# Kernel tuning notes

Hardware: AMD Instinct MI355X
Metric: run time of the kernel (lower is better)

## Reference

```python
import jax, jax.numpy as jnp
import numpy as np

W_PRIOR_STD = 1.0          # w_prior_stddev
OBS_STD = 1.0              # observational_noise_stddev
EPS = 1e-7                 # keras backend.epsilon()
B, E, K, C = 64, 32, 128, 512


def setup_inputs() -> dict:
    key = jax.random.key(0)
    k1, k2, k3, k4 = jax.random.split(key, 4)
    x = jax.random.normal(k1, (B, E, C), jnp.float32)
    prior_memory_mean = jax.random.normal(k2, (K, C), jnp.float32)  # truncated_normal(0,1) init
    prior_log_variance_scale = jax.random.uniform(k3, (), jnp.float32)  # scalar weight (init zeros; nonzero for testing)
    log_w_stddev = jnp.float32(0.3)  # constant(initial_w_stddev) init
    z_noise = jax.random.normal(k4, (E, B, C), jnp.float32)  # reparam noise for z_distribution.sample()
    return {"x": x, "prior_memory_mean": prior_memory_mean,
            "prior_log_variance_scale": prior_log_variance_scale,
            "log_w_stddev": log_w_stddev, "z_noise": z_noise}


def _kl_w(w, sw, k):
    # KL( N(w, sw^2 I_k) || N(0, w_prior^2 I_k) ), w_prior = 1
    return 0.5 * (k * sw * sw + jnp.sum(w * w, axis=-1) - k - 2.0 * k * jnp.log(sw))


def reference(x, prior_memory_mean, prior_log_variance_scale, log_w_stddev, z_noise):
    b, e, c = x.shape
    k = prior_memory_mean.shape[0]
    dt = x.dtype
    sw = jnp.exp(log_w_stddev)                      # w_stddev
    lam = (OBS_STD ** 2) / (W_PRIOR_STD ** 2)       # l2 regularizer in w-solve
    I_k = jnp.eye(k, dtype=dt)

    # prior state (tiled over batch)
    M0 = jnp.broadcast_to(prior_memory_mean[None], (b, k, c)) + jnp.zeros((b, k, c), dt)
    var = prior_log_variance_scale + EPS
    U0 = jnp.broadcast_to(var * I_k, (b, k, k)) + jnp.zeros((b, k, k), dt)

    z = jnp.transpose(x, (1, 0, 2))  # [E,B,C]

    def solve_w(M, z_t):
        # least squares: w = (M M^T + lam I)^{-1} M z  -> [B,K]
        A = jnp.einsum('bkc,blc->bkl', M, M) + lam * I_k
        rhs = jnp.einsum('bkc,bc->bk', M, z_t)
        return jnp.linalg.solve(A, rhs[..., None])[..., 0]

    def step(carry, z_t):
        M, U = carry                                    # [B,K,C], [B,K,K]
        w = solve_w(M, z_t)                             # memory sample == mean; iteration_count == 1
        delta = z_t - jnp.einsum('bk,bkc->bc', w, M)    # prediction delta [B,C]
        wU = jnp.einsum('bk,bkl->bl', w, U)             # cross variance [B,K]
        sigma = jnp.sum(wU * w, axis=-1) + OBS_STD ** 2 # z episode covariance [B]
        gain = wU / sigma[:, None]                      # [B,K]
        M_new = M + gain[..., None] * delta[:, None, :] # rank-1 Kalman update
        U_new = U - jnp.einsum('bk,bl->bkl', gain, wU)
        return (M_new, U_new), _kl_w(w, sw, k)          # per-step w divergence [B]

    (M_post, U_post), kl_episode = jax.lax.scan(step, (M0, U0), z)  # kl_episode [E,B]

    # read memory: batched solve with shared Gram matrix over episode
    A = jnp.einsum('bkc,blc->bkl', M_post, M_post) + lam * I_k
    rhs = jnp.einsum('bkc,ebc->bke', M_post, z)
    w_read = jnp.transpose(jnp.linalg.solve(A, rhs), (2, 0, 1))     # [E,B,K]
    z_mean = jnp.einsum('ebk,bkc->ebc', w_read, M_post)
    kl_read = _kl_w(w_read, sw, k)                                  # [E,B]

    total_divergence = jnp.mean(kl_episode + kl_read)               # add_loss value
    z_sample = z_mean + OBS_STD * z_noise                           # reparameterized sample
    return jnp.transpose(z_sample, (1, 0, 2)), total_divergence
```

## Files before the change

### kernel.cpp

```cpp
#include <hip/hip_runtime.h>

#define BB 64
#define EE 32
#define KK 128
#define CC 512
#define V0EPS 1e-7f

#define LTR 132
#define PTS 132
#define LKM 36
#define L36 36
#define LWT 176
#define SEG(i) ((((i) >> 4) * 20) + ((i) & 15))

#define SC_S2  0
#define SC_SIG 1
#define SC_KL  2
#define SC_B1  3
#define SC_B2  4
#define SC_R11 5
#define SC_R12 6
#define SC_R22 7

__device__ __forceinline__ float wsum64(float v) {
#pragma unroll
  for (int m = 32; m >= 1; m >>= 1) v += __shfl_xor(v, m, 64);
  return v;
}

__device__ __forceinline__ float wsum32(float v) {
#pragma unroll
  for (int m = 16; m >= 1; m >>= 1) v += __shfl_xor(v, m, 64);
  return v;
}

__device__ __forceinline__ float dot4(const float4 a, const float4 b) {
  return a.x * b.x + a.y * b.y + a.z * b.z + a.w * b.w;
}

__global__ __launch_bounds__(256) void a0_kernel(const float* __restrict__ M0,
                                                 float* __restrict__ wsA0) {
  __shared__ __align__(16) float sRow[CC];
  const int k = blockIdx.x >> 1, half = blockIdx.x & 1;
  for (int c = threadIdx.x; c < CC; c += 256) sRow[c] = M0[k * CC + c];
  __syncthreads();
  const int wv = threadIdx.x >> 6, ln = threadIdx.x & 63;
  const float4* zr = (const float4*)(sRow + 8 * ln);
  const float4 z0 = zr[0], z1 = zr[1];
  for (int li = 0; li < 16; ++li) {
    const int l = half * 64 + wv * 16 + li;
    const float4* rp = (const float4*)(M0 + l * CC + 8 * ln);
    const float4 a = rp[0], b = rp[1];
    float s = dot4(a, z0) + dot4(b, z1);
    s = wsum64(s);
    if (ln == 0) wsA0[k * KK + l] = s + (l == k ? 1.0f : 0.0f);
  }
}

__global__ __launch_bounds__(1024) void psinv_kernel(const float* __restrict__ x,
                                                     const float* __restrict__ M0,
                                                     float* __restrict__ wsP,
                                                     float* __restrict__ wsSp,
                                                     const float* __restrict__ A0g,
                                                     float* __restrict__ Ainv0) {
  __shared__ __align__(16) float zAll[32][520];
  __shared__ __align__(16) float Mch[2][16][520];
  __shared__ float sFb[2][128];
  __shared__ __align__(16) float sPv[2][256];
  __shared__ float sScal[2];
  const int tid = threadIdx.x;

  if (blockIdx.x > 0) {
    const int b = (blockIdx.x - 1) >> 2, kq = (blockIdx.x - 1) & 3;
    {
      const float4* x4 = (const float4*)(x + (size_t)b * EE * CC);
#pragma unroll
      for (int i = 0; i < 4; i++) {
        const int F = tid + 1024 * i, e = F >> 7, c4 = F & 127;
        ((float4*)zAll[e])[c4] = x4[F];
      }
    }
    const float4* M4 = (const float4*)M0;
    const int srow = tid >> 7, sc4 = tid & 127;
    const int kbase = kq * 32;
    float4 st0 = M4[(kbase + srow) * 128 + sc4];
    float4 st1 = M4[(kbase + 8 + srow) * 128 + sc4];
    int buf = 0;
    const int p = tid & 7;
    const int ep = (tid >> 3) & 15;
    const int kp = tid >> 7;
#pragma unroll 1
    for (int kc = 0; kc < 2; ++kc) {
      ((float4*)Mch[buf][srow])[sc4] = st0;
      ((float4*)Mch[buf][8 + srow])[sc4] = st1;
      __syncthreads();
      if (kc == 0) {
        st0 = M4[(kbase + 16 + srow) * 128 + sc4];
        st1 = M4[(kbase + 24 + srow) * 128 + sc4];
      }
      float s00 = 0, s01 = 0, s10 = 0, s11 = 0;
      const float* m0 = Mch[buf][kp];
      const float* m1 = Mch[buf][kp + 8];
      const float* z0 = zAll[2 * ep];
      const float* z1 = zAll[2 * ep + 1];
#pragma unroll
      for (int u = 0; u < 16; u++) {
        const int c = 4 * p + 32 * u;
        const float4 a0 = *(const float4*)(m0 + c);
        const float4 a1 = *(const float4*)(m1 + c);
        const float4 b0 = *(const float4*)(z0 + c);
        const float4 b1 = *(const float4*)(z1 + c);
        s00 += dot4(a0, b0); s01 += dot4(a0, b1);
        s10 += dot4(a1, b0); s11 += dot4(a1, b1);
      }
#pragma unroll
      for (int m = 1; m <= 4; m <<= 1) {
        s00 += __shfl_xor(s00, m, 64); s01 += __shfl_xor(s01, m, 64);
        s10 += __shfl_xor(s10, m, 64); s11 += __shfl_xor(s11, m, 64);
      }
      if (p == 0) {
        float* Pb = wsP + (size_t)b * KK * EE;
        Pb[(kbase + kc * 16 + kp) * EE + 2 * ep] = s00;
        Pb[(kbase + kc * 16 + kp) * EE + 2 * ep + 1] = s01;
        Pb[(kbase + kc * 16 + kp + 8) * EE + 2 * ep] = s10;
        Pb[(kbase + kc * 16 + kp + 8) * EE + 2 * ep + 1] = s11;
      }
      buf ^= 1;
    }
    {
      const int e = tid >> 5, f = tid & 31;
      const float4* ze = ((const float4*)zAll[e]) + 32 * kq;
      const float4* zf = ((const float4*)zAll[f]) + 32 * kq;
      float a0 = 0, a1 = 0, a2 = 0, a3 = 0;
#pragma unroll 4
      for (int u = 0; u < 32; u++) {
        const float4 A = ze[u], Bq = zf[u];
        a0 += A.x * Bq.x; a1 += A.y * Bq.y; a2 += A.z * Bq.z; a3 += A.w * Bq.w;
      }
      wsSp[((size_t)b * 4 + kq) * 1024 + e * EE + f] = (a0 + a1) + (a2 + a3);
    }
  } else {
    const int r = tid >> 3, q = tid & 7;
    float wreg[16], vreg[16];
    {
      const float4* a4 = (const float4*)(A0g + r * KK + 16 * q);
#pragma unroll
      for (int u = 0; u < 4; u++) {
        const float4 t4 = a4[u];
        wreg[4 * u] = t4.x; wreg[4 * u + 1] = t4.y; wreg[4 * u + 2] = t4.z; wreg[4 * u + 3] = t4.w;
      }
#pragma unroll
      for (int c = 0; c < 16; c++) vreg[c] = (16 * q + c == r) ? 1.0f : 0.0f;
    }
    if (q == 0) sFb[0][r] = wreg[0];
    if (r == 0) {
#pragma unroll
      for (int c = 0; c < 16; c++) { sPv[0][16 * q + c] = wreg[c]; sPv[0][128 + 16 * q + c] = vreg[c]; }
    }
    if (tid == 0) sScal[0] = 1.0f / wreg[0];
    __syncthreads();
#pragma unroll 1
    for (int j = 0; j < KK; ++j) {
      const int sl = j & 1, sn = sl ^ 1;
      const float f = sFb[sl][r] * sScal[sl];
      if (r != j) {
        if (16 * q + 15 >= j) {
          const float4* w4 = (const float4*)(sPv[sl] + 16 * q);
#pragma unroll
          for (int u = 0; u < 4; u++) {
            const float4 aa = w4[u];
            wreg[4 * u] -= f * aa.x; wreg[4 * u + 1] -= f * aa.y;
            wreg[4 * u + 2] -= f * aa.z; wreg[4 * u + 3] -= f * aa.w;
          }
        }
        if (16 * q <= j) {
          const float4* v4 = (const float4*)(sPv[sl] + 128 + 16 * q);
#pragma unroll
          for (int u = 0; u < 4; u++) {
            const float4 bb = v4[u];
            vreg[4 * u] -= f * bb.x; vreg[4 * u + 1] -= f * bb.y;
            vreg[4 * u + 2] -= f * bb.z; vreg[4 * u + 3] -= f * bb.w;
          }
        }
      }
      if (j + 1 < KK) {
        const int jn = j + 1;
        float wval = 0.0f;
#pragma unroll
        for (int c = 0; c < 16; c++) if (c == (jn & 15)) wval = wreg[c];
        if (q == (jn >> 4)) sFb[sn][r] = wval;
        if (r == jn) {
#pragma unroll
          for (int c = 0; c < 16; c++) { sPv[sn][16 * q + c] = wreg[c]; sPv[sn][128 + 16 * q + c] = vreg[c]; }
        }
        if (r == jn && q == (jn >> 4)) sScal[sn] = 1.0f / wval;
      }
      __syncthreads();
    }
    {
      float dval = 0.0f;
#pragma unroll
      for (int c = 0; c < 16; c++) if (c == (r & 15)) dval = wreg[c];
      if (q == (r >> 4)) sFb[0][r] = dval;
    }
    __syncthreads();
    {
      const float sc = 1.0f / sFb[0][r];
      float4* o4 = (float4*)(Ainv0 + r * KK + 16 * q);
#pragma unroll
      for (int u = 0; u < 4; u++) {
        float4 o;
        o.x = vreg[4 * u] * sc; o.y = vreg[4 * u + 1] * sc;
        o.z = vreg[4 * u + 2] * sc; o.w = vreg[4 * u + 3] * sc;
        o4[u] = o;
      }
    }
  }
}

__global__ __launch_bounds__(512) void scan_kernel(
    const float* __restrict__ Pg, const float* __restrict__ Sg,
    const float* __restrict__ scaleP, const float* __restrict__ Ainv0,
    float* __restrict__ wsKL, float* __restrict__ wsKLr, float* __restrict__ wsWt) {
  __shared__ __align__(16) float sPT[EE * PTS];
  __shared__ __align__(16) float sGT[EE * LTR];
  __shared__ __align__(16) float sEggT[EE * LTR];
  __shared__ __align__(16) float uni2[EE * LTR];
  __shared__ __align__(16) float uni3[KK * LKM];
  __shared__ __align__(16) float uni1[KK * LKM];
  __shared__ __align__(16) float sEk[KK * LKM];
  __shared__ __align__(16) float sS[EE * L36];
  __shared__ __align__(16) float sD[EE * L36];
  __shared__ __align__(16) float sW[160];
  __shared__ __align__(16) float sWU[160];
  __shared__ __align__(16) float sPu[160];
  __shared__ __align__(16) float sPm[160];
  __shared__ __align__(16) float sQ[160];
  __shared__ __align__(16) float sDz[EE];
  __shared__ __align__(16) float sDgw[EE];
  __shared__ __align__(16) float sQt[EE];
  __shared__ __align__(16) float sScal[16];

  float* sYT = uni2;
  float* sGk = uni3;
  float* sYk = uni1;

  const int tid = threadIdx.x, wv = tid >> 6, ln = tid & 63;
  const int mr = tid >> 2, mq = tid & 3;
  const int b = blockIdx.x;

  float areg[32];
  {
    const float4* a4 = (const float4*)(Ainv0 + mr * KK + 32 * mq);
#pragma unroll
    for (int u = 0; u < 8; u++) {
      const float4 t4 = a4[u];
      areg[4 * u] = t4.x; areg[4 * u + 1] = t4.y; areg[4 * u + 2] = t4.z; areg[4 * u + 3] = t4.w;
    }
  }
  {
    const float* Pb = Pg + (size_t)b * KK * EE;
#pragma unroll
    for (int i = 0; i < 8; i++) {
      const int idx = tid + 512 * i;
      sPT[(idx & 31) * PTS + (idx >> 5)] = Pb[idx];
    }
    const float* Sb = Sg + (size_t)b * 4096;
#pragma unroll
    for (int i = 0; i < 2; i++) {
      const int idx = tid + 512 * i;
      sS[(idx >> 5) * L36 + (idx & 31)] =
          Sb[idx] + Sb[idx + 1024] + Sb[idx + 2048] + Sb[idx + 3072];
    }
  }
  if (tid < 16) sScal[tid] = 0.0f;
  const float v0 = scaleP[0] + V0EPS;
  __syncthreads();
  {
    const float* xb = sPT + 32 * mq;
    float s = 0;
#pragma unroll
    for (int c = 0; c < 32; c++) s += areg[c] * xb[c];
    s += __shfl_xor(s, 1, 64); s += __shfl_xor(s, 2, 64);
    if (mq == 0) sW[SEG(mr)] = s;
  }
  __syncthreads();

#pragma unroll 1
  for (int t = 0; t < EE; ++t) {
    const bool hn = (t + 1 < EE);
    {
      const float* xb = sW + 40 * mq;
      float s = 0;
#pragma unroll
      for (int c = 0; c < 16; c++) s += areg[c] * xb[c];
#pragma unroll
      for (int c = 0; c < 16; c++) s += areg[16 + c] * xb[20 + c];
      s += __shfl_xor(s, 1, 64); s += __shfl_xor(s, 2, 64);
      if (mq == 0) sPm[SEG(mr)] = s;
    }
    if (tid < 256) {
      const int s8 = tid >> 3, p3 = tid & 7;
      if (s8 < t) {
        const float* gr = sGT + s8 * LTR + 16 * p3;
        const float* wr_ = sW + 20 * p3;
        float s = 0;
#pragma unroll
        for (int kk = 0; kk < 16; kk++) s += gr[kk] * wr_[kk];
        s += __shfl_xor(s, 1, 64); s += __shfl_xor(s, 2, 64); s += __shfl_xor(s, 4, 64);
        if (p3 == 0) sDgw[s8] = s;
      } else if (s8 == 31) {
        const float* wp = sW + 20 * p3;
        float s = 0;
#pragma unroll
        for (int kk = 0; kk < 16; kk++) s += wp[kk] * wp[kk];
        s += __shfl_xor(s, 1, 64); s += __shfl_xor(s, 2, 64); s += __shfl_xor(s, 4, 64);
        if (p3 == 0) sScal[SC_S2] = s;
      }
    } else {
      const int j = (tid - 256) >> 3, p3 = tid & 7;
      if (j < t) {
        const float* yr = sYT + j * LTR + 16 * p3;
        const float* wr_ = sW + 20 * p3;
        float s = 0;
#pragma unroll
        for (int kk = 0; kk < 16; kk++) s += yr[kk] * wr_[kk];
        s += __shfl_xor(s, 1, 64); s += __shfl_xor(s, 2, 64); s += __shfl_xor(s, 4, 64);
        if (p3 == 0) sQt[j] = s;
      }
    }
    __syncthreads();
    if (tid < 256) {
      const int k = tid >> 1, h = tid & 1;
      const float* yk = sYk + k * LKM + 16 * h;
      const float* qb = sQt + 16 * h;
      float a = 0;
#pragma unroll
      for (int u = 0; u < 16; u++) {
        const int j = 16 * h + u;
        a += (j < t) ? yk[u] * qb[u] : 0.0f;
      }
      a += __shfl_xor(a, 1, 64);
      if (h == 0) sWU[SEG(k)] = v0 * sW[SEG(k)] - a;
    } else if (tid < 384) {
      const int k = tid - 256;
      float a = sW[SEG(k)];
      const float* ek = sEk + k * LKM;
      const int nc = (t + 3) >> 2;
#pragma unroll 1
      for (int c4 = 0; c4 < nc; ++c4) {
        const float4 ev = *(const float4*)(ek + 4 * c4);
        const float4 dv = *(const float4*)(sDgw + 4 * c4);
        const int u0 = 4 * c4;
        a -= ((u0 + 0 < t) ? ev.x * dv.x : 0.0f) + ((u0 + 1 < t) ? ev.y * dv.y : 0.0f) +
             ((u0 + 2 < t) ? ev.z * dv.z : 0.0f) + ((u0 + 3 < t) ? ev.w * dv.w : 0.0f);
      }
      sEk[k * LKM + t] = a;
      sEggT[t * LTR + k] = a;
    } else if (tid < 448) {
      if (ln < 32) {
        const int r2 = ln;
        float a = (r2 == t) ? 1.0f : 0.0f;
        for (int s2 = 0; s2 < t; ++s2) a -= sDgw[s2] * sD[s2 * L36 + r2];
        sD[t * L36 + r2] = a;
      } else {
        const int k0 = (ln - 32) * 4;
        const float4 wv4 = *(const float4*)(sW + SEG(k0));
        const float4 pm4 = *(const float4*)(sPm + SEG(k0));
        float a = dot4(wv4, pm4);
        a = wsum32(a);
        if (ln == 32) sScal[SC_R22] = a;
      }
    } else {
      const float s2v = sScal[SC_S2];
      float a = (ln < t) ? sQt[ln] * sQt[ln] : 0.0f;
      a = wsum64(a);
      if (ln == 0) {
        sScal[SC_SIG] = v0 * s2v - a + 1.0f;
        sScal[SC_KL] += s2v;
      }
    }
    __syncthreads();
    {
      const float* xb = sWU + 40 * mq;
      float s = 0;
#pragma unroll
      for (int c = 0; c < 16; c++) s += areg[c] * xb[c];
#pragma unroll
      for (int c = 0; c < 16; c++) s += areg[16 + c] * xb[20 + c];
      s += __shfl_xor(s, 1, 64); s += __shfl_xor(s, 2, 64);
      if (mq == 0) sPu[SEG(mr)] = s;
    }
    if (tid < 256) {
      const int s4 = tid >> 3, p3 = tid & 7;
      if (hn && s4 <= t) {
        const float* er = sEggT + s4 * LTR + 16 * p3;
        const float* pr = sPT + (t + 1) * PTS + 16 * p3;
        float a = 0;
#pragma unroll
        for (int kk = 0; kk < 16; kk++) a -= er[kk] * pr[kk];
        const float4 dv = *(const float4*)(sD + s4 * L36 + 4 * p3);
        const float4 sv = *(const float4*)(sS + (t + 1) * L36 + 4 * p3);
        a += dot4(dv, sv);
        a += __shfl_xor(a, 1, 64); a += __shfl_xor(a, 2, 64); a += __shfl_xor(a, 4, 64);
        if (p3 == 0) sDz[s4] = a;
      }
    } else if (tid < 320) {
      float a = sEggT[t * LTR + ln] * sPT[t * PTS + ln] +
                sEggT[t * LTR + ln + 64] * sPT[t * PTS + ln + 64];
      a = wsum64(a);
      if (ln == 0) sScal[SC_B2] = a;
    } else if (tid < 384) {
      if (ln < 32) {
        float a = sD[t * L36 + ln] * sS[t * L36 + ln];
        a = wsum32(a);
        if (ln == 0) sScal[SC_B1] = a;
      } else {
        const int k0 = (ln - 32) * 4;
        const float4 wu4 = *(const float4*)(sWU + SEG(k0));
        const float4 pm4 = *(const float4*)(sPm + SEG(k0));
        float a = dot4(wu4, pm4);
        a = wsum32(a);
        if (ln == 32) sScal[SC_R12] = a;
      }
    } else if (tid < 448) {
      const float sig = sScal[SC_SIG];
      const float rsq = rsqrtf(sig);
#pragma unroll
      for (int u = 0; u < 2; u++) {
        const int k = ln + 64 * u;
        const float wu = sWU[SEG(k)];
        const float gv = wu / sig;
        const float yv = wu * rsq;
        sGT[t * LTR + k] = gv;
        sGk[k * LKM + t] = gv;
        sYT[t * LTR + k] = yv;
        sYk[k * LKM + t] = yv;
      }
    }
    __syncthreads();
    if (hn) {
      const float* gk = sGk + mr * LKM + 8 * mq;
      const float* dzb = sDz + 8 * mq;
      float a = 0;
#pragma unroll
      for (int u = 0; u < 8; u++) {
        const int s2 = 8 * mq + u;
        a += (s2 < t) ? gk[u] * dzb[u] : 0.0f;
      }
      a += __shfl_xor(a, 1, 64); a += __shfl_xor(a, 2, 64);
      if (mq == 0)
        sQ[SEG(mr)] = sPT[(t + 1) * PTS + mr] + a + (sWU[SEG(mr)] / sScal[SC_SIG]) * sDz[t];
    }
    if (wv == 0) {
      float a = sWU[SEG(ln)] * sPu[SEG(ln)] + sWU[SEG(ln + 64)] * sPu[SEG(ln + 64)];
      a = wsum64(a);
      if (ln == 0) sScal[SC_R11] = a;
    }
    __syncthreads();
    {
      const float4 sc0 = *(const float4*)(sScal);
      const float4 sc1 = *(const float4*)(sScal + 4);
      const float rs = 1.0f / sc0.y;
      const float beta = sc0.w - sc1.x - sc0.x;
      const float e11 = sc1.y * rs * rs;
      const float e12 = sc1.z * rs + 1.0f;
      const float e22 = sc1.w - beta;
      const float rd = 1.0f / (e11 * e22 - e12 * e12);
      const float t11 = e22 * rd, t12 = -e12 * rd, t22 = e11 * rd;
      const float u1r = sPu[SEG(mr)] * rs, u2r = sPm[SEG(mr)];
      const float* pub = sPu + 40 * mq;
      const float* pmb = sPm + 40 * mq;
#pragma unroll
      for (int c = 0; c < 16; c++) {
        const float u1c = pub[c] * rs;
        const float u2c = pmb[c];
        areg[c] -= u1r * (t11 * u1c + t12 * u2c) + u2r * (t12 * u1c + t22 * u2c);
      }
#pragma unroll
      for (int c = 0; c < 16; c++) {
        const float u1c = pub[20 + c] * rs;
        const float u2c = pmb[20 + c];
        areg[16 + c] -= u1r * (t11 * u1c + t12 * u2c) + u2r * (t12 * u1c + t22 * u2c);
      }
    }
    if (hn) {
      const float* xb = sQ + 40 * mq;
      float s = 0;
#pragma unroll
      for (int c = 0; c < 16; c++) s += areg[c] * xb[c];
#pragma unroll
      for (int c = 0; c < 16; c++) s += areg[16 + c] * xb[20 + c];
      s += __shfl_xor(s, 1, 64); s += __shfl_xor(s, 2, 64);
      if (mq == 0) sW[SEG(mr)] = s;
    }
    __syncthreads();
  }

  float* sR1T  = uni2;
  float* sGamT = uni2 + 1152;
  float* sRhsT = uni1;
  float* sWrT  = uni3;
  if (tid == 0) wsKL[b] = sScal[SC_KL];

#pragma unroll
  for (int h = 0; h < 2; ++h) {
    const int lin = tid + 512 * h, s = lin >> 5, e = lin & 31;
    const float4* er = (const float4*)(sEggT + s * LTR);
    const float4* pr = (const float4*)(sPT + e * PTS);
    float a = 0;
#pragma unroll 8
    for (int u = 0; u < 32; ++u) a -= dot4(er[u], pr[u]);
    const float4* dr = (const float4*)(sD + s * L36);
    const float4* sr = (const float4*)(sS + e * L36);
#pragma unroll
    for (int u = 0; u < 8; ++u) a += dot4(dr[u], sr[u]);
    sR1T[e * 36 + s] = a;
  }
  __syncthreads();
  {
    const int k = tid & 127, e4 = tid >> 7;
    float4 g0, g1, g2, g3, g4, g5, g6, g7;
    {
      const float4* gk = (const float4*)(sGk + k * LKM);
      g0 = gk[0]; g1 = gk[1]; g2 = gk[2]; g3 = gk[3];
      g4 = gk[4]; g5 = gk[5]; g6 = gk[6]; g7 = gk[7];
    }
#pragma unroll
    for (int u = 0; u < 8; ++u) {
      const int e = e4 * 8 + u;
      const float4* r1 = (const float4*)(sR1T + e * 36);
      float a = sPT[e * PTS + k];
      a += dot4(g0, r1[0]) + dot4(g1, r1[1]) + dot4(g2, r1[2]) + dot4(g3, r1[3]);
      a += dot4(g4, r1[4]) + dot4(g5, r1[5]) + dot4(g6, r1[6]) + dot4(g7, r1[7]);
      sRhsT[e * PTS + k] = a;
    }
  }
  __syncthreads();
#pragma unroll 2
  for (int e = 0; e < EE; ++e) {
    const float* xb = sRhsT + e * PTS + 32 * mq;
    float s = 0;
#pragma unroll
    for (int c = 0; c < 32; c++) s += areg[c] * xb[c];
    s += __shfl_xor(s, 1, 64); s += __shfl_xor(s, 2, 64);
    if (mq == 0) sWrT[e * PTS + mr] = s;
  }
  __syncthreads();
#pragma unroll
  for (int h = 0; h < 2; ++h) {
    const int lin = tid + 512 * h, s = lin >> 5, e = lin & 31;
    const float4* gr = (const float4*)(sGT + s * LTR);
    const float4* wr = (const float4*)(sWrT + e * PTS);
    float a = 0;
#pragma unroll 8
    for (int u = 0; u < 32; ++u) a += dot4(gr[u], wr[u]);
    sGamT[e * 36 + s] = a;
  }
  __syncthreads();
  {
    const int k = tid & 127, e4 = tid >> 7;
    float4 E0, E1, E2, E3, E4, E5, E6, E7;
    {
      const float4* ek = (const float4*)(sEk + k * LKM);
      E0 = ek[0]; E1 = ek[1]; E2 = ek[2]; E3 = ek[3];
      E4 = ek[4]; E5 = ek[5]; E6 = ek[6]; E7 = ek[7];
    }
#pragma unroll
    for (int u = 0; u < 8; ++u) {
      const int e = e4 * 8 + u;
      const float4* gm = (const float4*)(sGamT + e * 36);
      float a = sWrT[e * PTS + k];
      a -= dot4(E0, gm[0]) + dot4(E1, gm[1]) + dot4(E2, gm[2]) + dot4(E3, gm[3]);
      a -= dot4(E4, gm[4]) + dot4(E5, gm[5]) + dot4(E6, gm[6]) + dot4(E7, gm[7]);
      wsWt[(size_t)b * 5120 + e * 160 + k] = a;
    }
  }
  {
    const int e = tid & 31, sp = tid >> 5;
    float4 gm[8];
    {
      const float4* g4 = (const float4*)(sGamT + e * 36);
#pragma unroll
      for (int u = 0; u < 8; ++u) gm[u] = g4[u];
    }
#pragma unroll
    for (int h = 0; h < 2; ++h) {
      const int sp2 = sp + 16 * h;
      float a = 0;
#pragma unroll
      for (int u = 0; u < 8; ++u) {
        const float4 g = gm[u];
        a += sD[(4 * u + 0) * L36 + sp2] * g.x + sD[(4 * u + 1) * L36 + sp2] * g.y +
             sD[(4 * u + 2) * L36 + sp2] * g.z + sD[(4 * u + 3) * L36 + sp2] * g.w;
      }
      wsWt[(size_t)b * 5120 + e * 160 + 128 + sp2] = a;
    }
  }
  {
    const int e = tid >> 4, p = tid & 15;
    const float4* wr = (const float4*)(sWrT + e * PTS + 8 * p);
    const float4 w0 = wr[0], w1 = wr[1];
    float a = dot4(w0, w0) + dot4(w1, w1);
    a += __shfl_xor(a, 1, 64); a += __shfl_xor(a, 2, 64);
    a += __shfl_xor(a, 4, 64); a += __shfl_xor(a, 8, 64);
    if (p == 0) wsKLr[b * EE + e] = a;
  }
}

__global__ __launch_bounds__(512) void postBF_kernel(
    const float* __restrict__ wsWt, const float* __restrict__ x,
    const float* __restrict__ M0, const float* __restrict__ znoise,
    const float* __restrict__ wsKL, const float* __restrict__ wsKLr,
    const float* __restrict__ lwsP, float* __restrict__ out) {
  __shared__ __align__(16) float sWtT[32 * LWT];
  __shared__ __align__(16) float Mch[2 * 16 * 132];
  const int tid = threadIdx.x;

  if (blockIdx.x == 256) {
    float* sPp = sWtT;
    float s = 0.0f;
    if (tid < 64) s += wsKL[tid];
    for (int i = tid; i < 2048; i += 512) s += wsKLr[i];
    sPp[tid] = s;
    __syncthreads();
    for (int off = 256; off > 0; off >>= 1) {
      if (tid < off) sPp[tid] += sPp[tid + off];
      __syncthreads();
    }
    if (tid == 0) {
      const float lws = lwsP[0];
      const float sw2 = expf(2.0f * lws);
      out[(size_t)BB * EE * CC] =
          0.5f * sPp[0] / (float)(EE * BB) + (float)KK * (sw2 - 1.0f - 2.0f * lws);
    }
    return;
  }

  const int b = blockIdx.x >> 2, cq = blockIdx.x & 3;
  {
    const int e = tid >> 4, j = tid & 15;
    const float* Wg = wsWt + (size_t)b * 5120 + e * 160;
#pragma unroll
    for (int u = 0; u < 10; ++u) sWtT[e * LWT + j + 16 * u] = Wg[j + 16 * u];
  }
  const int srow = tid >> 5, sc4 = tid & 31;
  const int e = tid & 31, cs = tid >> 5;
  const float* xb = x + (size_t)b * EE * CC;
  const int cbase = cq * 128;
  float4 st = *(const float4*)(M0 + srow * CC + cbase + 4 * sc4);
  float acc[8];
#pragma unroll
  for (int u = 0; u < 8; u++) acc[u] = 0.0f;
  int buf = 0;
#pragma unroll 1
  for (int ch2 = 0; ch2 < 10; ++ch2) {
    *(float4*)(Mch + buf * 2112 + srow * 132 + 4 * sc4) = st;
    __syncthreads();
    if (ch2 + 1 < 10) {
      const int row = (ch2 + 1) * 16 + srow;
      st = (row < 128) ? *(const float4*)(M0 + row * CC + cbase + 4 * sc4)
                       : *(const float4*)(xb + (row - 128) * CC + cbase + 4 * sc4);
    }
    const float4* wt4 = (const float4*)(sWtT + e * LWT + ch2 * 16);
    const float4 wa = wt4[0], wb = wt4[1], wc = wt4[2], wd = wt4[3];
    const float wv16[16] = {wa.x, wa.y, wa.z, wa.w, wb.x, wb.y, wb.z, wb.w,
                            wc.x, wc.y, wc.z, wc.w, wd.x, wd.y, wd.z, wd.w};
#pragma unroll
    for (int kk = 0; kk < 16; ++kk) {
      const float* mrp = Mch + buf * 2112 + kk * 132 + cs * 8;
      const float4 m0 = *(const float4*)(mrp);
      const float4 m1 = *(const float4*)(mrp + 4);
      const float wk = wv16[kk];
      acc[0] += wk * m0.x; acc[1] += wk * m0.y; acc[2] += wk * m0.z; acc[3] += wk * m0.w;
      acc[4] += wk * m1.x; acc[5] += wk * m1.y; acc[6] += wk * m1.z; acc[7] += wk * m1.w;
    }
    buf ^= 1;
  }
  {
    const size_t ob = ((size_t)b * EE + e) * CC + cbase + cs * 8;
    const size_t nb = ((size_t)e * BB + b) * CC + cbase + cs * 8;
#pragma unroll
    for (int u = 0; u < 2; u++) {
      const float4 nz = *(const float4*)(znoise + nb + 4 * u);
      float4 o;
      o.x = acc[4 * u] + nz.x;     o.y = acc[4 * u + 1] + nz.y;
      o.z = acc[4 * u + 2] + nz.z; o.w = acc[4 * u + 3] + nz.w;
      *(float4*)(out + ob + 4 * u) = o;
    }
  }
}

extern "C" void kernel_launch(void* const* d_in, const int* in_sizes, int n_in,
                              void* d_out, int out_size, void* d_ws, size_t ws_size,
                              hipStream_t stream) {
  (void)in_sizes; (void)n_in; (void)out_size; (void)ws_size;
  const float* x = (const float*)d_in[0];
  const float* M0 = (const float*)d_in[1];
  const float* scaleP = (const float*)d_in[2];
  const float* lwsP = (const float*)d_in[3];
  const float* znoise = (const float*)d_in[4];
  float* out = (float*)d_out;

  float* ws = (float*)d_ws;
  float* wsP = ws;
  float* wsSp = wsP + 262144;
  float* wsA0 = wsSp + 262144;
  float* wsAinv0 = wsA0 + 16384;
  float* wsKL = wsAinv0 + 16384;
  float* wsKLr = wsKL + 64;
  float* wsWt = wsKLr + 2048;

  a0_kernel<<<256, 256, 0, stream>>>(M0, wsA0);
  psinv_kernel<<<257, 1024, 0, stream>>>(x, M0, wsP, wsSp, wsA0, wsAinv0);
  scan_kernel<<<BB, 512, 0, stream>>>(wsP, wsSp, scaleP, wsAinv0,
                                      wsKL, wsKLr, wsWt);
  postBF_kernel<<<257, 512, 0, stream>>>(wsWt, x, M0, znoise, wsKL, wsKLr, lwsP, out);
  final_kernel_dummy:;
}
```

Measured before the change: 289.2 us.

## Double scan kernel block to 1024 threads and repartition per-step phases

```diff
diff --git a/kernel.cpp b/kernel.cpp
--- a/kernel.cpp
+++ b/kernel.cpp
@@ -218,7 +218,7 @@
   }
 }
 
-__global__ __launch_bounds__(512) void scan_kernel(
+__global__ __launch_bounds__(1024) void scan_kernel(
     const float* __restrict__ Pg, const float* __restrict__ Sg,
     const float* __restrict__ scaleP, const float* __restrict__ Ainv0,
     float* __restrict__ wsKL, float* __restrict__ wsKLr, float* __restrict__ wsWt) {
@@ -245,12 +245,12 @@
   float* sGk = uni3;
   float* sYk = uni1;
 
-  const int tid = threadIdx.x, wv = tid >> 6, ln = tid & 63;
-  const int mr = tid >> 2, mq = tid & 3;
+  const int tid = threadIdx.x, ln = tid & 63;
+  const int mr = (tid >> 2) & 127, mq = tid & 3;
   const int b = blockIdx.x;
 
   float areg[32];
-  {
+  if (tid < 512) {
     const float4* a4 = (const float4*)(Ainv0 + mr * KK + 32 * mq);
 #pragma unroll
     for (int u = 0; u < 8; u++) {
@@ -261,22 +261,18 @@
   {
     const float* Pb = Pg + (size_t)b * KK * EE;
 #pragma unroll
-    for (int i = 0; i < 8; i++) {
-      const int idx = tid + 512 * i;
+    for (int i = 0; i < 4; i++) {
+      const int idx = tid + 1024 * i;
       sPT[(idx & 31) * PTS + (idx >> 5)] = Pb[idx];
     }
     const float* Sb = Sg + (size_t)b * 4096;
-#pragma unroll
-    for (int i = 0; i < 2; i++) {
-      const int idx = tid + 512 * i;
-      sS[(idx >> 5) * L36 + (idx & 31)] =
-          Sb[idx] + Sb[idx + 1024] + Sb[idx + 2048] + Sb[idx + 3072];
-    }
+    sS[(tid >> 5) * L36 + (tid & 31)] =
+        Sb[tid] + Sb[tid + 1024] + Sb[tid + 2048] + Sb[tid + 3072];
   }
   if (tid < 16) sScal[tid] = 0.0f;
   const float v0 = scaleP[0] + V0EPS;
   __syncthreads();
-  {
+  if (tid < 512) {
     const float* xb = sPT + 32 * mq;
     float s = 0;
 #pragma unroll
@@ -289,7 +285,7 @@
 #pragma unroll 1
   for (int t = 0; t < EE; ++t) {
     const bool hn = (t + 1 < EE);
-    {
+    if (tid < 512) {
       const float* xb = sW + 40 * mq;
       float s = 0;
 #pragma unroll
@@ -298,9 +294,8 @@
       for (int c = 0; c < 16; c++) s += areg[16 + c] * xb[20 + c];
       s += __shfl_xor(s, 1, 64); s += __shfl_xor(s, 2, 64);
       if (mq == 0) sPm[SEG(mr)] = s;
-    }
-    if (tid < 256) {
-      const int s8 = tid >> 3, p3 = tid & 7;
+    } else if (tid < 768) {
+      const int s8 = (tid - 512) >> 3, p3 = tid & 7;
       if (s8 < t) {
         const float* gr = sGT + s8 * LTR + 16 * p3;
         const float* wr_ = sW + 20 * p3;
@@ -318,7 +313,7 @@
         if (p3 == 0) sScal[SC_S2] = s;
       }
     } else {
-      const int j = (tid - 256) >> 3, p3 = tid & 7;
+      const int j = (tid - 768) >> 3, p3 = tid & 7;
       if (j < t) {
         const float* yr = sYT + j * LTR + 16 * p3;
         const float* wr_ = sW + 20 * p3;
@@ -343,7 +338,29 @@
       a += __shfl_xor(a, 1, 64);
       if (h == 0) sWU[SEG(k)] = v0 * sW[SEG(k)] - a;
     } else if (tid < 384) {
-      const int k = tid - 256;
+      const int r2 = (tid - 256) >> 2, p = tid & 3;
+      float a = 0;
+#pragma unroll
+      for (int u = 0; u < 8; u++) {
+        const int s2 = p + 4 * u;
+        a += (s2 < t) ? sDgw[s2] * sD[s2 * L36 + r2] : 0.0f;
+      }
+      a += __shfl_xor(a, 1, 64); a += __shfl_xor(a, 2, 64);
+      if (p == 0) sD[t * L36 + r2] = ((r2 == t) ? 1.0f : 0.0f) - a;
+    } else if (tid < 448) {
+      float a = sW[SEG(ln)] * sPm[SEG(ln)] + sW[SEG(ln + 64)] * sPm[SEG(ln + 64)];
+      a = wsum64(a);
+      if (ln == 0) sScal[SC_R22] = a;
+    } else if (tid < 512) {
+      const float s2v = sScal[SC_S2];
+      float a = (ln < t) ? sQt[ln] * sQt[ln] : 0.0f;
+      a = wsum64(a);
+      if (ln == 0) {
+        sScal[SC_SIG] = v0 * s2v - a + 1.0f;
+        sScal[SC_KL] += s2v;
+      }
+    } else if (tid < 640) {
+      const int k = tid - 512;
       float a = sW[SEG(k)];
       const float* ek = sEk + k * LKM;
       const int nc = (t + 3) >> 2;
@@ -357,43 +374,9 @@
       }
       sEk[k * LKM + t] = a;
       sEggT[t * LTR + k] = a;
-    } else if (tid < 448) {
-      if (ln < 32) {
-        const int r2 = ln;
-        float a = (r2 == t) ? 1.0f : 0.0f;
-        for (int s2 = 0; s2 < t; ++s2) a -= sDgw[s2] * sD[s2 * L36 + r2];
-        sD[t * L36 + r2] = a;
-      } else {
-        const int k0 = (ln - 32) * 4;
-        const float4 wv4 = *(const float4*)(sW + SEG(k0));
-        const float4 pm4 = *(const float4*)(sPm + SEG(k0));
-        float a = dot4(wv4, pm4);
-        a = wsum32(a);
-        if (ln == 32) sScal[SC_R22] = a;
-      }
-    } else {
-      const float s2v = sScal[SC_S2];
-      float a = (ln < t) ? sQt[ln] * sQt[ln] : 0.0f;
-      a = wsum64(a);
-      if (ln == 0) {
-        sScal[SC_SIG] = v0 * s2v - a + 1.0f;
-        sScal[SC_KL] += s2v;
-      }
-    }
-    __syncthreads();
-    {
-      const float* xb = sWU + 40 * mq;
-      float s = 0;
-#pragma unroll
-      for (int c = 0; c < 16; c++) s += areg[c] * xb[c];
-#pragma unroll
-      for (int c = 0; c < 16; c++) s += areg[16 + c] * xb[20 + c];
-      s += __shfl_xor(s, 1, 64); s += __shfl_xor(s, 2, 64);
-      if (mq == 0) sPu[SEG(mr)] = s;
-    }
-    if (tid < 256) {
-      const int s4 = tid >> 3, p3 = tid & 7;
-      if (hn && s4 <= t) {
+    } else if (tid < 896) {
+      const int s4 = (tid - 640) >> 3, p3 = tid & 7;
+      if (hn && s4 < t) {
         const float* er = sEggT + s4 * LTR + 16 * p3;
         const float* pr = sPT + (t + 1) * PTS + 16 * p3;
         float a = 0;
@@ -405,12 +388,31 @@
         a += __shfl_xor(a, 1, 64); a += __shfl_xor(a, 2, 64); a += __shfl_xor(a, 4, 64);
         if (p3 == 0) sDz[s4] = a;
       }
-    } else if (tid < 320) {
+    }
+    __syncthreads();
+    if (tid < 512) {
+      const float* xb = sWU + 40 * mq;
+      float s = 0;
+#pragma unroll
+      for (int c = 0; c < 16; c++) s += areg[c] * xb[c];
+#pragma unroll
+      for (int c = 0; c < 16; c++) s += areg[16 + c] * xb[20 + c];
+      s += __shfl_xor(s, 1, 64); s += __shfl_xor(s, 2, 64);
+      if (mq == 0) sPu[SEG(mr)] = s;
+    } else if (tid < 576) {
+      if (hn) {
+        float a = -(sEggT[t * LTR + ln] * sPT[(t + 1) * PTS + ln] +
+                    sEggT[t * LTR + ln + 64] * sPT[(t + 1) * PTS + ln + 64]);
+        if (ln < 32) a += sD[t * L36 + ln] * sS[(t + 1) * L36 + ln];
+        a = wsum64(a);
+        if (ln == 0) sDz[t] = a;
+      }
+    } else if (tid < 640) {
       float a = sEggT[t * LTR + ln] * sPT[t * PTS + ln] +
                 sEggT[t * LTR + ln + 64] * sPT[t * PTS + ln + 64];
       a = wsum64(a);
       if (ln == 0) sScal[SC_B2] = a;
-    } else if (tid < 384) {
+    } else if (tid < 704) {
       if (ln < 32) {
         float a = sD[t * L36 + ln] * sS[t * L36 + ln];
         a = wsum32(a);
@@ -423,7 +425,7 @@
         a = wsum32(a);
         if (ln == 32) sScal[SC_R12] = a;
       }
-    } else if (tid < 448) {
+    } else if (tid < 768) {
       const float sig = sScal[SC_SIG];
       const float rsq = rsqrtf(sig);
 #pragma unroll
@@ -439,60 +441,63 @@
       }
     }
     __syncthreads();
-    if (hn) {
-      const float* gk = sGk + mr * LKM + 8 * mq;
-      const float* dzb = sDz + 8 * mq;
-      float a = 0;
-#pragma unroll
-      for (int u = 0; u < 8; u++) {
-        const int s2 = 8 * mq + u;
-        a += (s2 < t) ? gk[u] * dzb[u] : 0.0f;
-      }
-      a += __shfl_xor(a, 1, 64); a += __shfl_xor(a, 2, 64);
-      if (mq == 0)
-        sQ[SEG(mr)] = sPT[(t + 1) * PTS + mr] + a + (sWU[SEG(mr)] / sScal[SC_SIG]) * sDz[t];
-    }
-    if (wv == 0) {
+    if (tid < 512) {
+      if (hn) {
+        const float* gk = sGk + mr * LKM + 8 * mq;
+        const float* dzb = sDz + 8 * mq;
+        float a = 0;
+#pragma unroll
+        for (int u = 0; u < 8; u++) {
+          const int s2 = 8 * mq + u;
+          a += (s2 < t) ? gk[u] * dzb[u] : 0.0f;
+        }
+        a += __shfl_xor(a, 1, 64); a += __shfl_xor(a, 2, 64);
+        if (mq == 0)
+          sQ[SEG(mr)] = sPT[(t + 1) * PTS + mr] + a + (sWU[SEG(mr)] / sScal[SC_SIG]) * sDz[t];
+      }
+    } else if (tid < 576) {
       float a = sWU[SEG(ln)] * sPu[SEG(ln)] + sWU[SEG(ln + 64)] * sPu[SEG(ln + 64)];
       a = wsum64(a);
       if (ln == 0) sScal[SC_R11] = a;
     }
     __syncthreads();
-    {
-      const float4 sc0 = *(const float4*)(sScal);
-      const float4 sc1 = *(const float4*)(sScal + 4);
-      const float rs = 1.0f / sc0.y;
-      const float beta = sc0.w - sc1.x - sc0.x;
-      const float e11 = sc1.y * rs * rs;
-      const float e12 = sc1.z * rs + 1.0f;
-      const float e22 = sc1.w - beta;
-      const float rd = 1.0f / (e11 * e22 - e12 * e12);
-      const float t11 = e22 * rd, t12 = -e12 * rd, t22 = e11 * rd;
-      const float u1r = sPu[SEG(mr)] * rs, u2r = sPm[SEG(mr)];
-      const float* pub = sPu + 40 * mq;
-      const float* pmb = sPm + 40 * mq;
-#pragma unroll
-      for (int c = 0; c < 16; c++) {
-        const float u1c = pub[c] * rs;
-        const float u2c = pmb[c];
-        areg[c] -= u1r * (t11 * u1c + t12 * u2c) + u2r * (t12 * u1c + t22 * u2c);
-      }
-#pragma unroll
-      for (int c = 0; c < 16; c++) {
-        const float u1c = pub[20 + c] * rs;
-        const float u2c = pmb[20 + c];
-        areg[16 + c] -= u1r * (t11 * u1c + t12 * u2c) + u2r * (t12 * u1c + t22 * u2c);
-      }
-    }
-    if (hn) {
-      const float* xb = sQ + 40 * mq;
-      float s = 0;
-#pragma unroll
-      for (int c = 0; c < 16; c++) s += areg[c] * xb[c];
-#pragma unroll
-      for (int c = 0; c < 16; c++) s += areg[16 + c] * xb[20 + c];
-      s += __shfl_xor(s, 1, 64); s += __shfl_xor(s, 2, 64);
-      if (mq == 0) sW[SEG(mr)] = s;
+    if (tid < 512) {
+      {
+        const float4 sc0 = *(const float4*)(sScal);
+        const float4 sc1 = *(const float4*)(sScal + 4);
+        const float rs = 1.0f / sc0.y;
+        const float beta = sc0.w - sc1.x - sc0.x;
+        const float e11 = sc1.y * rs * rs;
+        const float e12 = sc1.z * rs + 1.0f;
+        const float e22 = sc1.w - beta;
+        const float rd = 1.0f / (e11 * e22 - e12 * e12);
+        const float t11 = e22 * rd, t12 = -e12 * rd, t22 = e11 * rd;
+        const float u1r = sPu[SEG(mr)] * rs, u2r = sPm[SEG(mr)];
+        const float* pub = sPu + 40 * mq;
+        const float* pmb = sPm + 40 * mq;
+#pragma unroll
+        for (int c = 0; c < 16; c++) {
+          const float u1c = pub[c] * rs;
+          const float u2c = pmb[c];
+          areg[c] -= u1r * (t11 * u1c + t12 * u2c) + u2r * (t12 * u1c + t22 * u2c);
+        }
+#pragma unroll
+        for (int c = 0; c < 16; c++) {
+          const float u1c = pub[20 + c] * rs;
+          const float u2c = pmb[20 + c];
+          areg[16 + c] -= u1r * (t11 * u1c + t12 * u2c) + u2r * (t12 * u1c + t22 * u2c);
+        }
+      }
+      if (hn) {
+        const float* xb = sQ + 40 * mq;
+        float s = 0;
+#pragma unroll
+        for (int c = 0; c < 16; c++) s += areg[c] * xb[c];
+#pragma unroll
+        for (int c = 0; c < 16; c++) s += areg[16 + c] * xb[20 + c];
+        s += __shfl_xor(s, 1, 64); s += __shfl_xor(s, 2, 64);
+        if (mq == 0) sW[SEG(mr)] = s;
+      }
     }
     __syncthreads();
   }
@@ -503,9 +508,8 @@
   float* sWrT  = uni3;
   if (tid == 0) wsKL[b] = sScal[SC_KL];
 
-#pragma unroll
-  for (int h = 0; h < 2; ++h) {
-    const int lin = tid + 512 * h, s = lin >> 5, e = lin & 31;
+  {
+    const int s = tid >> 5, e = tid & 31;
     const float4* er = (const float4*)(sEggT + s * LTR);
     const float4* pr = (const float4*)(sPT + e * PTS);
     float a = 0;
@@ -519,7 +523,7 @@
   }
   __syncthreads();
   {
-    const int k = tid & 127, e4 = tid >> 7;
+    const int k = tid & 127, e8 = tid >> 7;
     float4 g0, g1, g2, g3, g4, g5, g6, g7;
     {
       const float4* gk = (const float4*)(sGk + k * LKM);
@@ -527,8 +531,8 @@
       g4 = gk[4]; g5 = gk[5]; g6 = gk[6]; g7 = gk[7];
     }
 #pragma unroll
-    for (int u = 0; u < 8; ++u) {
-      const int e = e4 * 8 + u;
+    for (int u = 0; u < 4; ++u) {
+      const int e = e8 * 4 + u;
       const float4* r1 = (const float4*)(sR1T + e * 36);
       float a = sPT[e * PTS + k];
       a += dot4(g0, r1[0]) + dot4(g1, r1[1]) + dot4(g2, r1[2]) + dot4(g3, r1[3]);
@@ -537,19 +541,20 @@
     }
   }
   __syncthreads();
+  if (tid < 512) {
 #pragma unroll 2
-  for (int e = 0; e < EE; ++e) {
-    const float* xb = sRhsT + e * PTS + 32 * mq;
-    float s = 0;
-#pragma unroll
-    for (int c = 0; c < 32; c++) s += areg[c] * xb[c];
-    s += __shfl_xor(s, 1, 64); s += __shfl_xor(s, 2, 64);
-    if (mq == 0) sWrT[e * PTS + mr] = s;
+    for (int e = 0; e < EE; ++e) {
+      const float* xb = sRhsT + e * PTS + 32 * mq;
+      float s = 0;
+#pragma unroll
+      for (int c = 0; c < 32; c++) s += areg[c] * xb[c];
+      s += __shfl_xor(s, 1, 64); s += __shfl_xor(s, 2, 64);
+      if (mq == 0) sWrT[e * PTS + mr] = s;
+    }
   }
   __syncthreads();
-#pragma unroll
-  for (int h = 0; h < 2; ++h) {
-    const int lin = tid + 512 * h, s = lin >> 5, e = lin & 31;
+  {
+    const int s = tid >> 5, e = tid & 31;
     const float4* gr = (const float4*)(sGT + s * LTR);
     const float4* wr = (const float4*)(sWrT + e * PTS);
     float a = 0;
@@ -559,7 +564,7 @@
   }
   __syncthreads();
   {
-    const int k = tid & 127, e4 = tid >> 7;
+    const int k = tid & 127, e8 = tid >> 7;
     float4 E0, E1, E2, E3, E4, E5, E6, E7;
     {
       const float4* ek = (const float4*)(sEk + k * LKM);
@@ -567,8 +572,8 @@
       E4 = ek[4]; E5 = ek[5]; E6 = ek[6]; E7 = ek[7];
     }
 #pragma unroll
-    for (int u = 0; u < 8; ++u) {
-      const int e = e4 * 8 + u;
+    for (int u = 0; u < 4; ++u) {
+      const int e = e8 * 4 + u;
       const float4* gm = (const float4*)(sGamT + e * 36);
       float a = sWrT[e * PTS + k];
       a -= dot4(E0, gm[0]) + dot4(E1, gm[1]) + dot4(E2, gm[2]) + dot4(E3, gm[3]);
@@ -584,27 +589,21 @@
 #pragma unroll
       for (int u = 0; u < 8; ++u) gm[u] = g4[u];
     }
-#pragma unroll
-    for (int h = 0; h < 2; ++h) {
-      const int sp2 = sp + 16 * h;
-      float a = 0;
-#pragma unroll
-      for (int u = 0; u < 8; ++u) {
-        const float4 g = gm[u];
-        a += sD[(4 * u + 0) * L36 + sp2] * g.x + sD[(4 * u + 1) * L36 + sp2] * g.y +
-             sD[(4 * u + 2) * L36 + sp2] * g.z + sD[(4 * u + 3) * L36 + sp2] * g.w;
-      }
-      wsWt[(size_t)b * 5120 + e * 160 + 128 + sp2] = a;
-    }
-  }
-  {
-    const int e = tid >> 4, p = tid & 15;
-    const float4* wr = (const float4*)(sWrT + e * PTS + 8 * p);
-    const float4 w0 = wr[0], w1 = wr[1];
-    float a = dot4(w0, w0) + dot4(w1, w1);
-    a += __shfl_xor(a, 1, 64); a += __shfl_xor(a, 2, 64);
-    a += __shfl_xor(a, 4, 64); a += __shfl_xor(a, 8, 64);
-    if (p == 0) wsKLr[b * EE + e] = a;
+    float a = 0;
+#pragma unroll
+    for (int u = 0; u < 8; ++u) {
+      const float4 g = gm[u];
+      a += sD[(4 * u + 0) * L36 + sp] * g.x + sD[(4 * u + 1) * L36 + sp] * g.y +
+           sD[(4 * u + 2) * L36 + sp] * g.z + sD[(4 * u + 3) * L36 + sp] * g.w;
+    }
+    wsWt[(size_t)b * 5120 + e * 160 + 128 + sp] = a;
+  }
+  {
+    const int e = tid >> 5, p = tid & 31;
+    const float4 w0 = *(const float4*)(sWrT + e * PTS + 4 * p);
+    float a = dot4(w0, w0);
+    a = wsum32(a);
+    if ((tid & 31) == 0) wsKLr[b * EE + e] = a;
   }
 }
 
@@ -713,8 +712,7 @@
 
   a0_kernel<<<256, 256, 0, stream>>>(M0, wsA0);
   psinv_kernel<<<257, 1024, 0, stream>>>(x, M0, wsP, wsSp, wsA0, wsAinv0);
-  scan_kernel<<<BB, 512, 0, stream>>>(wsP, wsSp, scaleP, wsAinv0,
-                                      wsKL, wsKLr, wsWt);
+  scan_kernel<<<BB, 1024, 0, stream>>>(wsP, wsSp, scaleP, wsAinv0,
+                                       wsKL, wsKLr, wsWt);
   postBF_kernel<<<257, 512, 0, stream>>>(wsWt, x, M0, znoise, wsKL, wsKLr, lwsP, out);
-  final_kernel_dummy:;
 }
```

New measurement: 287.9 us. Within noise of the previous version (-0.4%).

## Block Gauss-Jordan inversion two pivots per step and split A0 kernel finer

Applied to the files above, without the earlier changes.

```diff
diff --git a/kernel.cpp b/kernel.cpp
--- a/kernel.cpp
+++ b/kernel.cpp
@@ -41,14 +41,14 @@
 __global__ __launch_bounds__(256) void a0_kernel(const float* __restrict__ M0,
                                                  float* __restrict__ wsA0) {
   __shared__ __align__(16) float sRow[CC];
-  const int k = blockIdx.x >> 1, half = blockIdx.x & 1;
+  const int k = blockIdx.x >> 2, quarter = blockIdx.x & 3;
   for (int c = threadIdx.x; c < CC; c += 256) sRow[c] = M0[k * CC + c];
   __syncthreads();
   const int wv = threadIdx.x >> 6, ln = threadIdx.x & 63;
   const float4* zr = (const float4*)(sRow + 8 * ln);
   const float4 z0 = zr[0], z1 = zr[1];
-  for (int li = 0; li < 16; ++li) {
-    const int l = half * 64 + wv * 16 + li;
+  for (int li = 0; li < 8; ++li) {
+    const int l = quarter * 32 + wv * 8 + li;
     const float4* rp = (const float4*)(M0 + l * CC + 8 * ln);
     const float4 a = rp[0], b = rp[1];
     float s = dot4(a, z0) + dot4(b, z1);
@@ -65,9 +65,8 @@
                                                      float* __restrict__ Ainv0) {
   __shared__ __align__(16) float zAll[32][520];
   __shared__ __align__(16) float Mch[2][16][520];
-  __shared__ float sFb[2][128];
-  __shared__ __align__(16) float sPv[2][256];
-  __shared__ float sScal[2];
+  __shared__ __align__(16) float sFb[2][2][128];
+  __shared__ __align__(16) float sPv[2][2][256];
   const int tid = threadIdx.x;
 
   if (blockIdx.x > 0) {
@@ -152,48 +151,72 @@
 #pragma unroll
       for (int c = 0; c < 16; c++) vreg[c] = (16 * q + c == r) ? 1.0f : 0.0f;
     }
-    if (q == 0) sFb[0][r] = wreg[0];
+    if (q == 0) { sFb[0][0][r] = wreg[0]; sFb[0][1][r] = wreg[1]; }
     if (r == 0) {
 #pragma unroll
-      for (int c = 0; c < 16; c++) { sPv[0][16 * q + c] = wreg[c]; sPv[0][128 + 16 * q + c] = vreg[c]; }
-    }
-    if (tid == 0) sScal[0] = 1.0f / wreg[0];
+      for (int c = 0; c < 16; c++) { sPv[0][0][16 * q + c] = wreg[c]; sPv[0][0][128 + 16 * q + c] = vreg[c]; }
+    }
+    if (r == 1) {
+#pragma unroll
+      for (int c = 0; c < 16; c++) { sPv[0][1][16 * q + c] = wreg[c]; sPv[0][1][128 + 16 * q + c] = vreg[c]; }
+    }
     __syncthreads();
 #pragma unroll 1
-    for (int j = 0; j < KK; ++j) {
-      const int sl = j & 1, sn = sl ^ 1;
-      const float f = sFb[sl][r] * sScal[sl];
-      if (r != j) {
-        if (16 * q + 15 >= j) {
-          const float4* w4 = (const float4*)(sPv[sl] + 16 * q);
-#pragma unroll
-          for (int u = 0; u < 4; u++) {
-            const float4 aa = w4[u];
-            wreg[4 * u] -= f * aa.x; wreg[4 * u + 1] -= f * aa.y;
-            wreg[4 * u + 2] -= f * aa.z; wreg[4 * u + 3] -= f * aa.w;
-          }
+    for (int jj = 0; jj < 64; ++jj) {
+      const int j = 2 * jj, db = jj & 1, dn = db ^ 1;
+      const float* c0 = sFb[db][0];
+      const float* c1 = sFb[db][1];
+      const float* rj = sPv[db][0];
+      const float* rj1 = sPv[db][1];
+      const float p00 = c0[j], p10 = c0[j + 1], p01 = c1[j], p11 = c1[j + 1];
+      const float rp00 = 1.0f / p00;
+      const float g = p10 * rp00;
+      const float rp11 = 1.0f / (p11 - g * p01);
+      const float alpha = (r == j) ? 0.0f : c0[r] * rp00;
+      const float beta = (r == j + 1) ? 0.0f : (c1[r] - alpha * p01) * rp11;
+      const float ca = alpha - beta * g, cb = beta;
+      if (16 * q + 15 >= j) {
+        const float4* w0 = (const float4*)(rj + 16 * q);
+        const float4* w1 = (const float4*)(rj1 + 16 * q);
+#pragma unroll
+        for (int u = 0; u < 4; u++) {
+          const float4 a0 = w0[u], a1 = w1[u];
+          wreg[4 * u]     -= ca * a0.x + cb * a1.x;
+          wreg[4 * u + 1] -= ca * a0.y + cb * a1.y;
+          wreg[4 * u + 2] -= ca * a0.z + cb * a1.z;
+          wreg[4 * u + 3] -= ca * a0.w + cb * a1.w;
         }
-        if (16 * q <= j) {
-          const float4* v4 = (const float4*)(sPv[sl] + 128 + 16 * q);
-#pragma unroll
-          for (int u = 0; u < 4; u++) {
-            const float4 bb = v4[u];
-            vreg[4 * u] -= f * bb.x; vreg[4 * u + 1] -= f * bb.y;
-            vreg[4 * u + 2] -= f * bb.z; vreg[4 * u + 3] -= f * bb.w;
-          }
+      }
+      if (16 * q <= j + 1) {
+        const float4* v0 = (const float4*)(rj + 128 + 16 * q);
+        const float4* v1 = (const float4*)(rj1 + 128 + 16 * q);
+#pragma unroll
+        for (int u = 0; u < 4; u++) {
+          const float4 a0 = v0[u], a1 = v1[u];
+          vreg[4 * u]     -= ca * a0.x + cb * a1.x;
+          vreg[4 * u + 1] -= ca * a0.y + cb * a1.y;
+          vreg[4 * u + 2] -= ca * a0.z + cb * a1.z;
+          vreg[4 * u + 3] -= ca * a0.w + cb * a1.w;
         }
       }
-      if (j + 1 < KK) {
-        const int jn = j + 1;
-        float wval = 0.0f;
-#pragma unroll
-        for (int c = 0; c < 16; c++) if (c == (jn & 15)) wval = wreg[c];
-        if (q == (jn >> 4)) sFb[sn][r] = wval;
-        if (r == jn) {
-#pragma unroll
-          for (int c = 0; c < 16; c++) { sPv[sn][16 * q + c] = wreg[c]; sPv[sn][128 + 16 * q + c] = vreg[c]; }
+      if (jj + 1 < 64) {
+        const int j2 = j + 2, j3 = j + 3;
+        float w2 = 0.0f, w3 = 0.0f;
+#pragma unroll
+        for (int c = 0; c < 16; c++) {
+          if (c == (j2 & 15)) w2 = wreg[c];
+          if (c == (j3 & 15)) w3 = wreg[c];
         }
-        if (r == jn && q == (jn >> 4)) sScal[sn] = 1.0f / wval;
+        if (q == (j2 >> 4)) sFb[dn][0][r] = w2;
+        if (q == (j3 >> 4)) sFb[dn][1][r] = w3;
+        if (r == j2) {
+#pragma unroll
+          for (int c = 0; c < 16; c++) { sPv[dn][0][16 * q + c] = wreg[c]; sPv[dn][0][128 + 16 * q + c] = vreg[c]; }
+        }
+        if (r == j3) {
+#pragma unroll
+          for (int c = 0; c < 16; c++) { sPv[dn][1][16 * q + c] = wreg[c]; sPv[dn][1][128 + 16 * q + c] = vreg[c]; }
+        }
       }
       __syncthreads();
     }
@@ -201,11 +224,11 @@
       float dval = 0.0f;
 #pragma unroll
       for (int c = 0; c < 16; c++) if (c == (r & 15)) dval = wreg[c];
-      if (q == (r >> 4)) sFb[0][r] = dval;
-    }
-    __syncthreads();
-    {
-      const float sc = 1.0f / sFb[0][r];
+      if (q == (r >> 4)) sFb[0][0][r] = dval;
+    }
+    __syncthreads();
+    {
+      const float sc = 1.0f / sFb[0][0][r];
       float4* o4 = (float4*)(Ainv0 + r * KK + 16 * q);
 #pragma unroll
       for (int u = 0; u < 4; u++) {
@@ -711,10 +734,9 @@
   float* wsKLr = wsKL + 64;
   float* wsWt = wsKLr + 2048;
 
-  a0_kernel<<<256, 256, 0, stream>>>(M0, wsA0);
+  a0_kernel<<<512, 256, 0, stream>>>(M0, wsA0);
   psinv_kernel<<<257, 1024, 0, stream>>>(x, M0, wsP, wsSp, wsA0, wsAinv0);
   scan_kernel<<<BB, 512, 0, stream>>>(wsP, wsSp, scaleP, wsAinv0,
                                       wsKL, wsKLr, wsWt);
   postBF_kernel<<<257, 512, 0, stream>>>(wsWt, x, M0, znoise, wsKL, wsKLr, lwsP, out);
-  final_kernel_dummy:;
 }
```

After: 268.5 us. 1.08x faster.
